# Kernel tuning notes

Measured on AMD Instinct MI355X. Metric: run time of the kernel, lower is better.

The kernel has to match this reference:

```python
import jax, jax.numpy as jnp
import numpy as np

N = 100_000      # nodes
E = 1_600_000    # edges (avg degree 16)
D_IN = 128
D_H = 128
D_P = 128
D_OUT = 64


def setup_inputs() -> dict:
    key = jax.random.key(0)
    ks = jax.random.split(key, 10)
    x = jax.random.normal(ks[0], (N, D_IN), dtype=jnp.float32)
    edge_index = jax.random.randint(ks[1], (2, E), 0, N, dtype=jnp.int64)
    # Mix_Pass layer 0: Linear(in->hidden, bias=False) + separate bias (zero-init)
    W1 = jax.random.normal(ks[2], (D_H, D_IN), dtype=jnp.float32) * 0.05
    b1 = jnp.zeros((D_H,), dtype=jnp.float32)
    # Mix_Pass layer 1: hidden->hidden
    W2 = jax.random.normal(ks[3], (D_H, D_H), dtype=jnp.float32) * 0.05
    b2 = jnp.zeros((D_H,), dtype=jnp.float32)
    # projection MLP
    fcW1 = jax.random.normal(ks[4], (D_P, D_H), dtype=jnp.float32) * 0.05
    fcb1 = jnp.zeros((D_P,), dtype=jnp.float32)
    fcW2 = jax.random.normal(ks[5], (D_OUT, D_P), dtype=jnp.float32) * 0.05
    fcb2 = jnp.zeros((D_OUT,), dtype=jnp.float32)
    return dict(x=x, edge_index=edge_index, W1=W1, b1=b1, W2=W2, b2=b2,
                fcW1=fcW1, fcb1=fcb1, fcW2=fcW2, fcb2=fcb2)


def _gcn_norm_with_self_loops(edge_index, n_nodes):
    # add_self_loops then gcn_norm (sym, improved=False, loops already added)
    loop = jnp.arange(n_nodes, dtype=edge_index.dtype)
    row = jnp.concatenate([edge_index[0], loop])  # source
    col = jnp.concatenate([edge_index[1], loop])  # target
    ew = jnp.ones(row.shape[0], dtype=jnp.float32)
    deg = jax.ops.segment_sum(ew, col, num_segments=n_nodes)
    dinv = jnp.where(deg > 0, jax.lax.rsqrt(deg), 0.0)
    return row, col, dinv[row] * ew * dinv[col]


def _mix_pass(z, W, b, row, col, ew, n_nodes):
    z = z @ W.T                                   # [N, out]
    msg = ew[:, None] * z[row]                    # gather source feats, scale
    out = jax.ops.segment_sum(msg, col, num_segments=n_nodes)  # scatter-add
    return out + b


def reference(x, edge_index, W1, b1, W2, b2, fcW1, fcb1, fcW2, fcb2):
    n_nodes = x.shape[0]
    row, col, ew = _gcn_norm_with_self_loops(edge_index, n_nodes)
    # dropout is identity in eval mode
    z = jax.nn.relu(_mix_pass(x, W1, b1, row, col, ew, n_nodes))
    zs = _mix_pass(z, W2, b2, row, col, ew, n_nodes)
    # project: elu(fc1) -> log_softmax(fc2)
    h = jax.nn.elu(zs @ fcW1.T + fcb1)
    res = jax.nn.log_softmax(h @ fcW2.T + fcb2, axis=1)
    return zs, res
```

## Files before the change

kernel.cpp:

```cpp
#include <hip/hip_runtime.h>
#include <hip/hip_bf16.h>

typedef __bf16 bf16_t;
typedef bf16_t bf16x8 __attribute__((ext_vector_type(8)));
typedef bf16_t bf16x4 __attribute__((ext_vector_type(4)));
typedef bf16_t bf16x2 __attribute__((ext_vector_type(2)));
typedef float f32x4 __attribute__((ext_vector_type(4)));
typedef float f32x2 __attribute__((ext_vector_type(2)));

#define DEG_CAP 64
#define BKT_SHIFT 8
#define BKT_CAP 6144
#define EPT 16

__device__ __forceinline__ void cvt4(const float* __restrict__ s, bf16_t* __restrict__ d, int i) {
    f32x4 v = ((const f32x4*)s)[i];
    bf16x4 o;
#pragma unroll
    for (int j = 0; j < 4; ++j) o[j] = (bf16_t)v[j];
    ((bf16x4*)d)[i] = o;
}

__global__ void setup_k(const float* W1f, bf16_t* W1b,
                        const float* W2f, bf16_t* W2b,
                        const float* fW1f, bf16_t* fW1b,
                        const float* fW2f, bf16_t* fW2b,
                        int* gbcnt, int NB, int* yzero) {
    int i = blockIdx.x * blockDim.x + threadIdx.x;
    if (i < 4096) { cvt4(W1f, W1b, i); return; }
    i -= 4096;
    if (i < 4096) { cvt4(W2f, W2b, i); return; }
    i -= 4096;
    if (i < 4096) { cvt4(fW1f, fW1b, i); return; }
    i -= 4096;
    if (i < 2048) { cvt4(fW2f, fW2b, i); return; }
    i -= 2048;
    if (i < NB) { gbcnt[i] = 0; return; }
    i -= NB;
    if (i < 64) yzero[i] = 0;
}

__global__ __launch_bounds__(256) void bucket_scatter_k(const int* __restrict__ ei,
                                                        int* __restrict__ gbcnt,
                                                        unsigned* __restrict__ grec,
                                                        int E, int N) {
    __shared__ int hist[512];
    __shared__ int base[512];
    const int tid = threadIdx.x;
    const int NB = (N + 255) >> BKT_SHIFT;
    for (int i = tid; i < NB; i += 256) hist[i] = 0;
    __syncthreads();

    const int wave = tid >> 6, lane = tid & 63;
    const int e0 = blockIdx.x * (256 * EPT) + wave * (64 * EPT) + lane;
    const bool i64 = (ei[1] == 0) & (ei[3] == 0) & (ei[5] == 0) & (ei[7] == 0);

    unsigned rec[EPT];
    int lof[EPT];
    int bk[EPT];
#pragma unroll
    for (int j = 0; j < EPT; ++j) {
        int e = e0 + j * 64;
        bk[j] = -1;
        if (e < E) {
            int r, c;
            if (i64) { r = ei[2 * e]; c = ei[2 * E + 2 * e]; }
            else     { r = ei[e];     c = ei[E + e]; }
            r = ((unsigned)r < (unsigned)N) ? r : 0;
            c = ((unsigned)c < (unsigned)N) ? c : 0;
            int b = c >> BKT_SHIFT;
            rec[j] = ((unsigned)r << BKT_SHIFT) | (unsigned)(c & 255);
            bk[j] = b;
            lof[j] = atomicAdd(&hist[b], 1);
        }
    }
    __syncthreads();
    for (int i = tid; i < NB; i += 256)
        base[i] = hist[i] ? atomicAdd(&gbcnt[i], hist[i]) : 0;
    __syncthreads();
#pragma unroll
    for (int j = 0; j < EPT; ++j) {
        if (bk[j] >= 0) {
            int pos = base[bk[j]] + lof[j];
            if (pos < BKT_CAP)
                grec[(size_t)bk[j] * BKT_CAP + pos] = rec[j];
        }
    }
}

__global__ __launch_bounds__(256) void bucket_place_k(const int* __restrict__ gbcnt,
                                                      const unsigned* __restrict__ grec,
                                                      int* __restrict__ cnt,
                                                      int* __restrict__ srcx, int N) {
    __shared__ int lcnt[256];
    const int b = blockIdx.x, tid = threadIdx.x;
    lcnt[tid] = 0;
    __syncthreads();
    int ne = gbcnt[b];
    if (ne > BKT_CAP) ne = BKT_CAP;
    const unsigned* rp = grec + (size_t)b * BKT_CAP;
    const int node0 = b << BKT_SHIFT;
    for (int i = tid; i < ne; i += 256) {
        unsigned rec = rp[i];
        int cl = rec & 255;
        int r  = rec >> BKT_SHIFT;
        int p = atomicAdd(&lcnt[cl], 1);
        if (p < DEG_CAP) srcx[(size_t)(node0 + cl) * DEG_CAP + p] = r;
    }
    __syncthreads();
    int node = node0 + tid;
    if (node < N) {
        int c = lcnt[tid];
        cnt[node] = c;
        int cc = (c < DEG_CAP) ? c : DEG_CAP;
        int pe = (cc + 15) & ~15;
        if (pe < 16) pe = 16;
        if (pe > DEG_CAP) pe = DEG_CAP;
        int* s = srcx + (size_t)node * DEG_CAP;
        for (int p = cc; p < pe; ++p) s[p] = N;
    }
}

template <int RELU, int WF32>
__global__ __launch_bounds__(256) void gather_k(const bf16_t* __restrict__ Y,
                                                const int* __restrict__ cnt,
                                                const int* __restrict__ srcx,
                                                const float* __restrict__ bias,
                                                bf16_t* __restrict__ out,
                                                float* __restrict__ out2, int n) {
    int node = blockIdx.x * 4 + (threadIdx.x >> 6);
    if (node >= n) return;
    const int lane = threadIdx.x & 63;
    const int l16 = lane & 15;
    const int quad = lane >> 4;
    const int* sl = srcx + (size_t)node * DEG_CAP + quad * 4;
    const bf16_t* Yl = Y + l16 * 8;

    int4 sq = *(const int4*)sl;
    bf16x8 ys = *(const bf16x8*)(Yl + (size_t)node * 128);
    int c = cnt[node];
    float di = rsqrtf((float)c + 1.0f);
    int cg = (c < DEG_CAP) ? c : DEG_CAP;
    int nb = (cg + 15) & ~15;

    f32x2 acc[4];
#pragma unroll
    for (int p = 0; p < 4; ++p) acc[p] = (f32x2){0.f, 0.f};

#define ACC_ROW(s)                                                             \
    {                                                                          \
        bf16x8 yv = *(const bf16x8*)(Yl + (size_t)(s) * 128);                  \
        uint4 u = *(const uint4*)&yv;                                          \
        acc[0] += (f32x2){__uint_as_float(u.x << 16),                          \
                          __uint_as_float(u.x & 0xFFFF0000u)};                 \
        acc[1] += (f32x2){__uint_as_float(u.y << 16),                          \
                          __uint_as_float(u.y & 0xFFFF0000u)};                 \
        acc[2] += (f32x2){__uint_as_float(u.z << 16),                          \
                          __uint_as_float(u.z & 0xFFFF0000u)};                 \
        acc[3] += (f32x2){__uint_as_float(u.w << 16),                          \
                          __uint_as_float(u.w & 0xFFFF0000u)};                 \
    }

    ACC_ROW(sq.x); ACC_ROW(sq.y); ACC_ROW(sq.z); ACC_ROW(sq.w);
    for (int e = 16; e < nb; e += 16) {
        int4 s2 = *(const int4*)(sl + e);
        ACC_ROW(s2.x); ACC_ROW(s2.y); ACC_ROW(s2.z); ACC_ROW(s2.w);
    }
#undef ACC_ROW

    float a[8];
#pragma unroll
    for (int p = 0; p < 4; ++p) { a[2 * p] = acc[p][0]; a[2 * p + 1] = acc[p][1]; }
#pragma unroll
    for (int j = 0; j < 8; ++j) {
        a[j] += __shfl_xor(a[j], 16);
        a[j] += __shfl_xor(a[j], 32);
    }

    f32x4 b0 = ((const f32x4*)bias)[l16 * 2];
    f32x4 b1 = ((const f32x4*)bias)[l16 * 2 + 1];
    float v[8];
#pragma unroll
    for (int j = 0; j < 8; ++j) {
        float bb = (j < 4) ? b0[j & 3] : b1[j & 3];
        v[j] = di * ((float)ys[j] + a[j]) + bb;
        if (RELU) v[j] = fmaxf(v[j], 0.f);
    }

    if (quad == 0) {
        bf16x8 o;
#pragma unroll
        for (int j = 0; j < 8; ++j) o[j] = (bf16_t)v[j];
        *(bf16x8*)(out + (size_t)node * 128 + l16 * 8) = o;
    }
    if (WF32) {
        if (quad == 1) {
            f32x4 w = {v[0], v[1], v[2], v[3]};
            *(f32x4*)(out2 + (size_t)node * 128 + l16 * 8) = w;
        } else if (quad == 2) {
            f32x4 w = {v[4], v[5], v[6], v[7]};
            *(f32x4*)(out2 + (size_t)node * 128 + l16 * 8 + 4) = w;
        }
    }
}

template <int OC, int MT, int AF32>
__global__ __launch_bounds__(256) void gemm_k(const void* __restrict__ Av,
                                              const bf16_t* __restrict__ W,
                                              const int* __restrict__ cnt,
                                              bf16_t* __restrict__ out, int nrows) {
    const int lane = threadIdx.x & 63;
    const int wave = threadIdx.x >> 6;
    const int l16 = lane & 15;
    const int quad = lane >> 4;
    constexpr int NT = OC / 16;
    const int ntiles = (nrows + 15) >> 4;
    const int t0 = (blockIdx.x * 4 + wave) * MT;
    if (t0 >= ntiles) return;

    f32x4 acc[MT][NT];
#pragma unroll
    for (int mt = 0; mt < MT; ++mt)
#pragma unroll
        for (int n = 0; n < NT; ++n) acc[mt][n] = (f32x4){0.f, 0.f, 0.f, 0.f};

    const bf16_t* arow[MT];
    const float* afrow[MT];
#pragma unroll
    for (int mt = 0; mt < MT; ++mt) {
        int r = t0 * 16 + mt * 16 + l16;
        if (r > nrows - 1) r = nrows - 1;
        if (AF32) afrow[mt] = (const float*)Av + (size_t)r * 128 + quad * 8;
        else      arow[mt]  = (const bf16_t*)Av + (size_t)r * 128 + quad * 8;
    }
    const bf16_t* wrow = W + (size_t)l16 * 128 + quad * 8;

#pragma unroll
    for (int kt = 0; kt < 4; ++kt) {
        bf16x8 a[MT];
#pragma unroll
        for (int mt = 0; mt < MT; ++mt) {
            if (AF32) {
                f32x4 lo = *(const f32x4*)(afrow[mt] + kt * 32);
                f32x4 hi = *(const f32x4*)(afrow[mt] + kt * 32 + 4);
#pragma unroll
                for (int j = 0; j < 4; ++j) {
                    a[mt][j] = (bf16_t)lo[j];
                    a[mt][j + 4] = (bf16_t)hi[j];
                }
            } else {
                a[mt] = *(const bf16x8*)(arow[mt] + kt * 32);
            }
        }
#pragma unroll
        for (int n = 0; n < NT; ++n) {
            bf16x8 b = *(const bf16x8*)(wrow + (size_t)n * 2048 + kt * 32);
#pragma unroll
            for (int mt = 0; mt < MT; ++mt)
                acc[mt][n] = __builtin_amdgcn_mfma_f32_16x16x32_bf16(a[mt], b, acc[mt][n], 0, 0, 0);
        }
    }

#pragma unroll
    for (int mt = 0; mt < MT; ++mt) {
        int m0 = (t0 + mt) * 16;
        if (m0 >= nrows) break;
#pragma unroll
        for (int r = 0; r < 4; ++r) {
            int row = m0 + quad * 4 + r;
            if (row < nrows) {
                float sc = rsqrtf((float)cnt[row] + 1.0f);
#pragma unroll
                for (int n = 0; n < NT; ++n)
                    out[(size_t)row * OC + n * 16 + l16] = (bf16_t)(sc * acc[mt][n][r]);
            }
        }
    }
}

#define LDW 136
__global__ __launch_bounds__(256) void head_k(const bf16_t* __restrict__ A,
                                              const bf16_t* __restrict__ W1,
                                              const float* __restrict__ b1,
                                              const bf16_t* __restrict__ W2,
                                              const float* __restrict__ b2,
                                              float* __restrict__ outf, int nrows) {
    __shared__ bf16_t hl[4][16 * LDW];
    const int lane = threadIdx.x & 63;
    const int wave = threadIdx.x >> 6;
    const int l16 = lane & 15;
    const int quad = lane >> 4;
    const int ntiles = (nrows + 15) >> 4;
    int t = blockIdx.x * 4 + wave;
    const bool live = t < ntiles;
    if (!live) t = ntiles - 1;
    const int m0 = t * 16;

    f32x4 acc[8];
#pragma unroll
    for (int n = 0; n < 8; ++n) acc[n] = (f32x4){0.f, 0.f, 0.f, 0.f};
    int r0 = m0 + l16;
    if (r0 > nrows - 1) r0 = nrows - 1;
    const bf16_t* arow = A + (size_t)r0 * 128 + quad * 8;
    const bf16_t* wrow = W1 + (size_t)l16 * 128 + quad * 8;
#pragma unroll
    for (int kt = 0; kt < 4; ++kt) {
        bf16x8 a = *(const bf16x8*)(arow + kt * 32);
#pragma unroll
        for (int n = 0; n < 8; ++n) {
            bf16x8 b = *(const bf16x8*)(wrow + (size_t)n * 2048 + kt * 32);
            acc[n] = __builtin_amdgcn_mfma_f32_16x16x32_bf16(a, b, acc[n], 0, 0, 0);
        }
    }
    bf16_t* hw = hl[wave];
#pragma unroll
    for (int n = 0; n < 8; ++n) {
        float bb = b1[n * 16 + l16];
#pragma unroll
        for (int r = 0; r < 4; ++r) {
            float v = acc[n][r] + bb;
            v = (v > 0.0f) ? v : (expf(v) - 1.0f);
            hw[(quad * 4 + r) * LDW + n * 16 + l16] = (bf16_t)v;
        }
    }
    __syncthreads();

    f32x4 acc2[4];
#pragma unroll
    for (int n = 0; n < 4; ++n) acc2[n] = (f32x4){0.f, 0.f, 0.f, 0.f};
    const bf16_t* hrow = hw + l16 * LDW + quad * 8;
    const bf16_t* wrow2 = W2 + (size_t)l16 * 128 + quad * 8;
#pragma unroll
    for (int kt = 0; kt < 4; ++kt) {
        bf16x8 a = *(const bf16x8*)(hrow + kt * 32);
#pragma unroll
        for (int n = 0; n < 4; ++n) {
            bf16x8 b = *(const bf16x8*)(wrow2 + (size_t)n * 2048 + kt * 32);
            acc2[n] = __builtin_amdgcn_mfma_f32_16x16x32_bf16(a, b, acc2[n], 0, 0, 0);
        }
    }
#pragma unroll
    for (int r = 0; r < 4; ++r) {
        float v[4];
#pragma unroll
        for (int n = 0; n < 4; ++n) v[n] = acc2[n][r] + b2[n * 16 + l16];
        float mx = v[0];
#pragma unroll
        for (int n = 1; n < 4; ++n) mx = fmaxf(mx, v[n]);
#pragma unroll
        for (int m = 8; m >= 1; m >>= 1) mx = fmaxf(mx, __shfl_xor(mx, m));
        float s = 0.0f;
#pragma unroll
        for (int n = 0; n < 4; ++n) s += expf(v[n] - mx);
#pragma unroll
        for (int m = 8; m >= 1; m >>= 1) s += __shfl_xor(s, m);
        float lse = mx + logf(s);
        int row = m0 + quad * 4 + r;
        if (live && row < nrows)
#pragma unroll
            for (int n = 0; n < 4; ++n)
                outf[(size_t)row * 64 + n * 16 + l16] = v[n] - lse;
    }
}

extern "C" void kernel_launch(void* const* d_in, const int* in_sizes, int n_in,
                              void* d_out, int out_size, void* d_ws, size_t ws_size,
                              hipStream_t stream) {
    const float* xf    = (const float*)d_in[0];
    const int*   ei    = (const int*)d_in[1];
    const float* W1f   = (const float*)d_in[2];
    const float* b1f   = (const float*)d_in[3];
    const float* W2f   = (const float*)d_in[4];
    const float* b2f   = (const float*)d_in[5];
    const float* fcW1f = (const float*)d_in[6];
    const float* fcb1f = (const float*)d_in[7];
    const float* fcW2f = (const float*)d_in[8];
    const float* fcb2f = (const float*)d_in[9];

    const int N = in_sizes[0] / 128;
    const int E = in_sizes[1] / 2;
    const int NB = (N + 255) >> BKT_SHIFT;

    float* zs_out  = (float*)d_out;
    float* res_out = (float*)d_out + (size_t)N * 128;

    char* ws = (char*)d_ws;
    size_t o = 0;
    auto carve = [&](size_t bytes) { void* p = ws + o; o = (o + bytes + 255) & ~255UL; return p; };
    int*      cnt   = (int*)carve((size_t)N * 4);
    int*      srcx  = (int*)carve((size_t)N * DEG_CAP * 4);
    bf16_t*   Xbf   = (bf16_t*)carve((size_t)N * 128 * 2);
    bf16_t*   Ybf   = (bf16_t*)carve((size_t)(N + 1) * 128 * 2);
    bf16_t*   W1b   = (bf16_t*)carve(128 * 128 * 2);
    bf16_t*   W2b   = (bf16_t*)carve(128 * 128 * 2);
    bf16_t*   fW1b  = (bf16_t*)carve(128 * 128 * 2);
    bf16_t*   fW2b  = (bf16_t*)carve(64 * 128 * 2);
    unsigned* grec  = (unsigned*)carve((size_t)NB * BKT_CAP * 4);
    int*      gbcnt = (int*)carve((size_t)NB * 4);

    const int B = 256;
    const int ntiles = (N + 15) / 16;
    const int gblocks = (ntiles + 7) / 8;
    const int hblocks = (ntiles + 3) / 4;
    const int nodeblocks = (N + 3) / 4;
    const int nsetup = 4096 * 3 + 2048 + NB + 64;
    const int ablocks = (E + 256 * EPT - 1) / (256 * EPT);

    setup_k<<<(nsetup + B - 1) / B, B, 0, stream>>>(W1f, W1b, W2f, W2b,
                                                    fcW1f, fW1b, fcW2f, fW2b, gbcnt, NB,
                                                    (int*)(Ybf + (size_t)N * 128));
    bucket_scatter_k<<<ablocks, B, 0, stream>>>(ei, gbcnt, grec, E, N);
    bucket_place_k<<<NB, B, 0, stream>>>(gbcnt, grec, cnt, srcx, N);

    gemm_k<128, 2, 1><<<gblocks, B, 0, stream>>>((const void*)xf, W1b, cnt, Ybf, N);
    gather_k<1, 0><<<nodeblocks, B, 0, stream>>>(Ybf, cnt, srcx, b1f, Xbf, nullptr, N);

    gemm_k<128, 2, 0><<<gblocks, B, 0, stream>>>((const void*)Xbf, W2b, cnt, Ybf, N);
    gather_k<0, 1><<<nodeblocks, B, 0, stream>>>(Ybf, cnt, srcx, b2f, Xbf, zs_out, N);

    head_k<<<hblocks, B, 0, stream>>>(Xbf, fW1b, fcb1f, fW2b, fcb2f, res_out, N);
}
```

Before: 394.6 us.

## Fuse gather with next GEMM and gather with projection head

The layer-1 gather is merged with the layer-2 GEMM (W2) into one 1024-thread kernel, and the layer-2 gather is merged with the projection MLP and log_softmax. Each block gathers 16 nodes into shared memory and then runs the MFMA on that tile. This removes the bf16 intermediate round trips through global memory and two kernel launches. In exchange it uses large blocks with a barrier between gather and GEMM, and only 8 or 1 of the 16 waves do the matmul, which may hurt occupancy and latency hiding.

```diff
diff --git a/kernel.cpp b/kernel.cpp
--- a/kernel.cpp
+++ b/kernel.cpp
@@ -4,7 +4,6 @@
 typedef __bf16 bf16_t;
 typedef bf16_t bf16x8 __attribute__((ext_vector_type(8)));
 typedef bf16_t bf16x4 __attribute__((ext_vector_type(4)));
-typedef bf16_t bf16x2 __attribute__((ext_vector_type(2)));
 typedef float f32x4 __attribute__((ext_vector_type(4)));
 typedef float f32x2 __attribute__((ext_vector_type(2)));
 
@@ -12,6 +11,7 @@
 #define BKT_SHIFT 8
 #define BKT_CAP 6144
 #define EPT 16
+#define LDW 136
 
 __device__ __forceinline__ void cvt4(const float* __restrict__ s, bf16_t* __restrict__ d, int i) {
     f32x4 v = ((const f32x4*)s)[i];
@@ -25,7 +25,7 @@
                         const float* W2f, bf16_t* W2b,
                         const float* fW1f, bf16_t* fW1b,
                         const float* fW2f, bf16_t* fW2b,
-                        int* gbcnt, int NB, int* yzero) {
+                        int* gbcnt, int NB, int* yzero, int* xzero) {
     int i = blockIdx.x * blockDim.x + threadIdx.x;
     if (i < 4096) { cvt4(W1f, W1b, i); return; }
     i -= 4096;
@@ -37,7 +37,9 @@
     i -= 2048;
     if (i < NB) { gbcnt[i] = 0; return; }
     i -= NB;
-    if (i < 64) yzero[i] = 0;
+    if (i < 64) { yzero[i] = 0; return; }
+    i -= 64;
+    if (i < 64) xzero[i] = 0;
 }
 
 __global__ __launch_bounds__(256) void bucket_scatter_k(const int* __restrict__ ei,
@@ -121,22 +123,16 @@
     }
 }
 
-template <int RELU, int WF32>
-__global__ __launch_bounds__(256) void gather_k(const bf16_t* __restrict__ Y,
-                                                const int* __restrict__ cnt,
-                                                const int* __restrict__ srcx,
-                                                const float* __restrict__ bias,
-                                                bf16_t* __restrict__ out,
-                                                float* __restrict__ out2, int n) {
-    int node = blockIdx.x * 4 + (threadIdx.x >> 6);
-    if (node >= n) return;
-    const int lane = threadIdx.x & 63;
-    const int l16 = lane & 15;
-    const int quad = lane >> 4;
+template <int RELU>
+__device__ __forceinline__ void gather_v(const bf16_t* __restrict__ Y,
+                                         const int* __restrict__ cnt,
+                                         const int* __restrict__ srcx,
+                                         const float* __restrict__ bias,
+                                         int node, int l16, int quad, float* v) {
     const int* sl = srcx + (size_t)node * DEG_CAP + quad * 4;
     const bf16_t* Yl = Y + l16 * 8;
 
-    int4 sq = *(const int4*)sl;
+    int4 sq0 = *(const int4*)sl;
     bf16x8 ys = *(const bf16x8*)(Yl + (size_t)node * 128);
     int c = cnt[node];
     float di = rsqrtf((float)c + 1.0f);
@@ -161,7 +157,7 @@
                           __uint_as_float(u.w & 0xFFFF0000u)};                 \
     }
 
-    ACC_ROW(sq.x); ACC_ROW(sq.y); ACC_ROW(sq.z); ACC_ROW(sq.w);
+    ACC_ROW(sq0.x); ACC_ROW(sq0.y); ACC_ROW(sq0.z); ACC_ROW(sq0.w);
     for (int e = 16; e < nb; e += 16) {
         int4 s2 = *(const int4*)(sl + e);
         ACC_ROW(s2.x); ACC_ROW(s2.y); ACC_ROW(s2.z); ACC_ROW(s2.w);
@@ -179,27 +175,149 @@
 
     f32x4 b0 = ((const f32x4*)bias)[l16 * 2];
     f32x4 b1 = ((const f32x4*)bias)[l16 * 2 + 1];
-    float v[8];
 #pragma unroll
     for (int j = 0; j < 8; ++j) {
         float bb = (j < 4) ? b0[j & 3] : b1[j & 3];
         v[j] = di * ((float)ys[j] + a[j]) + bb;
         if (RELU) v[j] = fmaxf(v[j], 0.f);
     }
-
-    if (quad == 0) {
-        bf16x8 o;
-#pragma unroll
-        for (int j = 0; j < 8; ++j) o[j] = (bf16_t)v[j];
-        *(bf16x8*)(out + (size_t)node * 128 + l16 * 8) = o;
-    }
-    if (WF32) {
-        if (quad == 1) {
+}
+
+__global__ __launch_bounds__(1024) void gg_k(const bf16_t* __restrict__ Y,
+                                             const int* __restrict__ cnt,
+                                             const int* __restrict__ srcx,
+                                             const float* __restrict__ b1,
+                                             const bf16_t* __restrict__ W2,
+                                             bf16_t* __restrict__ out, int n) {
+    __shared__ bf16_t at[16][LDW];
+    const int wave = threadIdx.x >> 6;
+    const int lane = threadIdx.x & 63;
+    const int l16 = lane & 15;
+    const int quad = lane >> 4;
+    const int node = blockIdx.x * 16 + wave;
+
+    if (node < n) {
+        float v[8];
+        gather_v<1>(Y, cnt, srcx, b1, node, l16, quad, v);
+        if (quad == 0) {
+            bf16x8 o;
+#pragma unroll
+            for (int j = 0; j < 8; ++j) o[j] = (bf16_t)v[j];
+            *(bf16x8*)&at[wave][l16 * 8] = o;
+        }
+    }
+    __syncthreads();
+
+    if (wave < 8) {
+        f32x4 acc = (f32x4){0.f, 0.f, 0.f, 0.f};
+        const bf16_t* wr = W2 + (size_t)(wave * 16 + l16) * 128 + quad * 8;
+#pragma unroll
+        for (int kt = 0; kt < 4; ++kt) {
+            bf16x8 a = *(const bf16x8*)&at[l16][kt * 32 + quad * 8];
+            bf16x8 b = *(const bf16x8*)(wr + kt * 32);
+            acc = __builtin_amdgcn_mfma_f32_16x16x32_bf16(a, b, acc, 0, 0, 0);
+        }
+#pragma unroll
+        for (int r = 0; r < 4; ++r) {
+            int row = blockIdx.x * 16 + quad * 4 + r;
+            if (row < n) {
+                float sc = rsqrtf((float)cnt[row] + 1.0f);
+                out[(size_t)row * 128 + wave * 16 + l16] = (bf16_t)(sc * acc[r]);
+            }
+        }
+    }
+}
+
+__global__ __launch_bounds__(1024) void gh_k(const bf16_t* __restrict__ Y,
+                                             const int* __restrict__ cnt,
+                                             const int* __restrict__ srcx,
+                                             const float* __restrict__ b2,
+                                             float* __restrict__ zs_out,
+                                             const bf16_t* __restrict__ fW1,
+                                             const float* __restrict__ fb1,
+                                             const bf16_t* __restrict__ fW2,
+                                             const float* __restrict__ fb2,
+                                             float* __restrict__ res_out, int n) {
+    __shared__ bf16_t zt[16][LDW];
+    __shared__ bf16_t ht[16][LDW];
+    const int wave = threadIdx.x >> 6;
+    const int lane = threadIdx.x & 63;
+    const int l16 = lane & 15;
+    const int quad = lane >> 4;
+    const int node = blockIdx.x * 16 + wave;
+
+    if (node < n) {
+        float v[8];
+        gather_v<0>(Y, cnt, srcx, b2, node, l16, quad, v);
+        if (quad == 0) {
+            bf16x8 o;
+#pragma unroll
+            for (int j = 0; j < 8; ++j) o[j] = (bf16_t)v[j];
+            *(bf16x8*)&zt[wave][l16 * 8] = o;
+        } else if (quad == 1) {
             f32x4 w = {v[0], v[1], v[2], v[3]};
-            *(f32x4*)(out2 + (size_t)node * 128 + l16 * 8) = w;
+            *(f32x4*)(zs_out + (size_t)node * 128 + l16 * 8) = w;
         } else if (quad == 2) {
             f32x4 w = {v[4], v[5], v[6], v[7]};
-            *(f32x4*)(out2 + (size_t)node * 128 + l16 * 8 + 4) = w;
+            *(f32x4*)(zs_out + (size_t)node * 128 + l16 * 8 + 4) = w;
+        }
+    }
+    __syncthreads();
+
+    if (wave < 8) {
+        f32x4 acc = (f32x4){0.f, 0.f, 0.f, 0.f};
+        const bf16_t* wr = fW1 + (size_t)(wave * 16 + l16) * 128 + quad * 8;
+#pragma unroll
+        for (int kt = 0; kt < 4; ++kt) {
+            bf16x8 a = *(const bf16x8*)&zt[l16][kt * 32 + quad * 8];
+            bf16x8 b = *(const bf16x8*)(wr + kt * 32);
+            acc = __builtin_amdgcn_mfma_f32_16x16x32_bf16(a, b, acc, 0, 0, 0);
+        }
+        float bb = fb1[wave * 16 + l16];
+#pragma unroll
+        for (int r = 0; r < 4; ++r) {
+            float h = acc[r] + bb;
+            h = (h > 0.0f) ? h : (expf(h) - 1.0f);
+            ht[quad * 4 + r][wave * 16 + l16] = (bf16_t)h;
+        }
+    }
+    __syncthreads();
+
+    if (wave == 0) {
+        f32x4 acc2[4];
+#pragma unroll
+        for (int m = 0; m < 4; ++m) acc2[m] = (f32x4){0.f, 0.f, 0.f, 0.f};
+        const bf16_t* wr2 = fW2 + (size_t)l16 * 128 + quad * 8;
+#pragma unroll
+        for (int kt = 0; kt < 4; ++kt) {
+            bf16x8 a = *(const bf16x8*)&ht[l16][kt * 32 + quad * 8];
+#pragma unroll
+            for (int m = 0; m < 4; ++m) {
+                bf16x8 b = *(const bf16x8*)(wr2 + (size_t)m * 2048 + kt * 32);
+                acc2[m] = __builtin_amdgcn_mfma_f32_16x16x32_bf16(a, b, acc2[m], 0, 0, 0);
+            }
+        }
+#pragma unroll
+        for (int r = 0; r < 4; ++r) {
+            float v[4];
+#pragma unroll
+            for (int m = 0; m < 4; ++m) v[m] = acc2[m][r] + fb2[m * 16 + l16];
+            float mx = v[0];
+#pragma unroll
+            for (int m = 1; m < 4; ++m) mx = fmaxf(mx, v[m]);
+#pragma unroll
+            for (int s = 8; s >= 1; s >>= 1) mx = fmaxf(mx, __shfl_xor(mx, s));
+            float sum = 0.0f;
+#pragma unroll
+            for (int m = 0; m < 4; ++m) sum += expf(v[m] - mx);
+#pragma unroll
+            for (int s = 8; s >= 1; s >>= 1) sum += __shfl_xor(sum, s);
+            float lse = mx + logf(sum);
+            int row = blockIdx.x * 16 + quad * 4 + r;
+            if (row < n)
+#pragma unroll
+                for (int m = 0; m < 4; ++m)
+                    res_out[(size_t)row * 64 + m * 16 + l16] = v[m] - lse;
         }
     }
 }
@@ -278,91 +396,6 @@
     }
 }
 
-#define LDW 136
-__global__ __launch_bounds__(256) void head_k(const bf16_t* __restrict__ A,
-                                              const bf16_t* __restrict__ W1,
-                                              const float* __restrict__ b1,
-                                              const bf16_t* __restrict__ W2,
-                                              const float* __restrict__ b2,
-                                              float* __restrict__ outf, int nrows) {
-    __shared__ bf16_t hl[4][16 * LDW];
-    const int lane = threadIdx.x & 63;
-    const int wave = threadIdx.x >> 6;
-    const int l16 = lane & 15;
-    const int quad = lane >> 4;
-    const int ntiles = (nrows + 15) >> 4;
-    int t = blockIdx.x * 4 + wave;
-    const bool live = t < ntiles;
-    if (!live) t = ntiles - 1;
-    const int m0 = t * 16;
-
-    f32x4 acc[8];
-#pragma unroll
-    for (int n = 0; n < 8; ++n) acc[n] = (f32x4){0.f, 0.f, 0.f, 0.f};
-    int r0 = m0 + l16;
-    if (r0 > nrows - 1) r0 = nrows - 1;
-    const bf16_t* arow = A + (size_t)r0 * 128 + quad * 8;
-    const bf16_t* wrow = W1 + (size_t)l16 * 128 + quad * 8;
-#pragma unroll
-    for (int kt = 0; kt < 4; ++kt) {
-        bf16x8 a = *(const bf16x8*)(arow + kt * 32);
-#pragma unroll
-        for (int n = 0; n < 8; ++n) {
-            bf16x8 b = *(const bf16x8*)(wrow + (size_t)n * 2048 + kt * 32);
-            acc[n] = __builtin_amdgcn_mfma_f32_16x16x32_bf16(a, b, acc[n], 0, 0, 0);
-        }
-    }
-    bf16_t* hw = hl[wave];
-#pragma unroll
-    for (int n = 0; n < 8; ++n) {
-        float bb = b1[n * 16 + l16];
-#pragma unroll
-        for (int r = 0; r < 4; ++r) {
-            float v = acc[n][r] + bb;
-            v = (v > 0.0f) ? v : (expf(v) - 1.0f);
-            hw[(quad * 4 + r) * LDW + n * 16 + l16] = (bf16_t)v;
-        }
-    }
-    __syncthreads();
-
-    f32x4 acc2[4];
-#pragma unroll
-    for (int n = 0; n < 4; ++n) acc2[n] = (f32x4){0.f, 0.f, 0.f, 0.f};
-    const bf16_t* hrow = hw + l16 * LDW + quad * 8;
-    const bf16_t* wrow2 = W2 + (size_t)l16 * 128 + quad * 8;
-#pragma unroll
-    for (int kt = 0; kt < 4; ++kt) {
-        bf16x8 a = *(const bf16x8*)(hrow + kt * 32);
-#pragma unroll
-        for (int n = 0; n < 4; ++n) {
-            bf16x8 b = *(const bf16x8*)(wrow2 + (size_t)n * 2048 + kt * 32);
-            acc2[n] = __builtin_amdgcn_mfma_f32_16x16x32_bf16(a, b, acc2[n], 0, 0, 0);
-        }
-    }
-#pragma unroll
-    for (int r = 0; r < 4; ++r) {
-        float v[4];
-#pragma unroll
-        for (int n = 0; n < 4; ++n) v[n] = acc2[n][r] + b2[n * 16 + l16];
-        float mx = v[0];
-#pragma unroll
-        for (int n = 1; n < 4; ++n) mx = fmaxf(mx, v[n]);
-#pragma unroll
-        for (int m = 8; m >= 1; m >>= 1) mx = fmaxf(mx, __shfl_xor(mx, m));
-        float s = 0.0f;
-#pragma unroll
-        for (int n = 0; n < 4; ++n) s += expf(v[n] - mx);
-#pragma unroll
-        for (int m = 8; m >= 1; m >>= 1) s += __shfl_xor(s, m);
-        float lse = mx + logf(s);
-        int row = m0 + quad * 4 + r;
-        if (live && row < nrows)
-#pragma unroll
-            for (int n = 0; n < 4; ++n)
-                outf[(size_t)row * 64 + n * 16 + l16] = v[n] - lse;
-    }
-}
-
 extern "C" void kernel_launch(void* const* d_in, const int* in_sizes, int n_in,
                               void* d_out, int out_size, void* d_ws, size_t ws_size,
                               hipStream_t stream) {
@@ -389,7 +422,7 @@
     auto carve = [&](size_t bytes) { void* p = ws + o; o = (o + bytes + 255) & ~255UL; return p; };
     int*      cnt   = (int*)carve((size_t)N * 4);
     int*      srcx  = (int*)carve((size_t)N * DEG_CAP * 4);
-    bf16_t*   Xbf   = (bf16_t*)carve((size_t)N * 128 * 2);
+    bf16_t*   Xbf   = (bf16_t*)carve((size_t)(N + 1) * 128 * 2);
     bf16_t*   Ybf   = (bf16_t*)carve((size_t)(N + 1) * 128 * 2);
     bf16_t*   W1b   = (bf16_t*)carve(128 * 128 * 2);
     bf16_t*   W2b   = (bf16_t*)carve(128 * 128 * 2);
@@ -401,22 +434,21 @@
     const int B = 256;
     const int ntiles = (N + 15) / 16;
     const int gblocks = (ntiles + 7) / 8;
-    const int hblocks = (ntiles + 3) / 4;
-    const int nodeblocks = (N + 3) / 4;
-    const int nsetup = 4096 * 3 + 2048 + NB + 64;
+    const int fblocks = ntiles;
+    const int nsetup = 4096 * 3 + 2048 + NB + 128;
     const int ablocks = (E + 256 * EPT - 1) / (256 * EPT);
 
     setup_k<<<(nsetup + B - 1) / B, B, 0, stream>>>(W1f, W1b, W2f, W2b,
                                                     fcW1f, fW1b, fcW2f, fW2b, gbcnt, NB,
-                                                    (int*)(Ybf + (size_t)N * 128));
+                                                    (int*)(Ybf + (size_t)N * 128),
+                                                    (int*)(Xbf + (size_t)N * 128));
     bucket_scatter_k<<<ablocks, B, 0, stream>>>(ei, gbcnt, grec, E, N);
     bucket_place_k<<<NB, B, 0, stream>>>(gbcnt, grec, cnt, srcx, N);
 
     gemm_k<128, 2, 1><<<gblocks, B, 0, stream>>>((const void*)xf, W1b, cnt, Ybf, N);
-    gather_k<1, 0><<<nodeblocks, B, 0, stream>>>(Ybf, cnt, srcx, b1f, Xbf, nullptr, N);
-
-    gemm_k<128, 2, 0><<<gblocks, B, 0, stream>>>((const void*)Xbf, W2b, cnt, Ybf, N);
-    gather_k<0, 1><<<nodeblocks, B, 0, stream>>>(Ybf, cnt, srcx, b2f, Xbf, zs_out, N);
-
-    head_k<<<hblocks, B, 0, stream>>>(Xbf, fW1b, fcb1f, fW2b, fcb2f, res_out, N);
-}
+
+    gg_k<<<fblocks, 1024, 0, stream>>>(Ybf, cnt, srcx, b1f, W2b, Xbf, N);
+
+    gh_k<<<fblocks, 1024, 0, stream>>>(Xbf, cnt, srcx, b2f, zs_out,
+                                       fW1b, fcb1f, fW2b, fcb2f, res_out, N);
+}
```

Result: no change. 395.4 us (+0.2%).
